# Optimization experiments

Hardware: AMD Instinct MI355X
Metric: run time of the kernel (lower is better)

Reference implementation:

```python
import jax, jax.numpy as jnp
import numpy as np

B, N, N_FEAT = 16, 1024, 128
N_LAYER, AGG_HIDDEN, FC_HIDDEN, N_CLASS = 3, 64, 128, 10
NEG_INF = -9e15
LEAKY_SLOPE = 0.2


def setup_inputs() -> dict:
    key = jax.random.key(0)
    ks = jax.random.split(key, 8)
    x = jax.random.normal(ks[0], (B, N, N_FEAT), dtype=jnp.float32)
    adj = jax.random.randint(ks[1], (B, N, N), 0, 2).astype(jnp.float32)
    # per-layer GAT params, stacked over layers
    Ws = jax.random.normal(ks[2], (N_LAYER, N_FEAT, AGG_HIDDEN), dtype=jnp.float32) * 0.1
    a1 = jax.random.normal(ks[3], (N_LAYER, AGG_HIDDEN), dtype=jnp.float32) * 0.1
    a2 = jax.random.normal(ks[4], (N_LAYER, AGG_HIDDEN), dtype=jnp.float32) * 0.1
    W1 = jax.random.normal(ks[5], (AGG_HIDDEN * N_LAYER, FC_HIDDEN), dtype=jnp.float32) * 0.05
    b1 = jnp.zeros((FC_HIDDEN,), dtype=jnp.float32)
    W2 = jax.random.normal(ks[6], (FC_HIDDEN, N_CLASS), dtype=jnp.float32) * 0.05
    b2 = jnp.zeros((N_CLASS,), dtype=jnp.float32)
    return {"x": x, "adj": adj, "Ws": Ws, "a1": a1, "a2": a2,
            "W1": W1, "b1": b1, "W2": W2, "b2": b2}


def _gat_layer(x, adj, W, a1, a2):
    # h: [B, N, H]
    h = jnp.einsum('bnf,fh->bnh', x, W)
    # e_ij = LeakyReLU(a1.h_i + a2.h_j)  -- split-a trick, avoids [B,N,N,2H]
    f1 = jnp.einsum('bnh,h->bn', h, a1)
    f2 = jnp.einsum('bnh,h->bn', h, a2)
    e = jax.nn.leaky_relu(f1[:, :, None] + f2[:, None, :], LEAKY_SLOPE)  # [B,N,N]
    att = jax.nn.softmax(jnp.where(adj > 0, e, NEG_INF), axis=-1)
    return jnp.einsum('bnm,bmh->bnh', att, h)


def reference(x, adj, Ws, a1, a2, W1, b1, W2, b2):
    # eval mode: dropout is identity
    outs = [jax.nn.relu(_gat_layer(x, adj, Ws[i], a1[i], a2[i]))
            for i in range(N_LAYER)]
    h = jnp.concatenate(outs, axis=2)          # [B, N, H*L]
    pooled = jnp.mean(h, axis=1)               # 'avg' pool over nodes -> [B, H*L]
    z = jax.nn.relu(pooled @ W1 + b1)
    return jax.nn.softmax(z @ W2 + b2, axis=-1)  # [B, n_class]
```

## Files before the change

kernel.cpp:

```cpp
#include <hip/hip_runtime.h>

#define B 16
#define N 1024
#define NF 128
#define NL 3
#define AH 64
#define HC 192
#define FCH 128
#define NC 10
#define L2E 1.44269504088896f

typedef __attribute__((ext_vector_type(8))) short bf16x8;
typedef __attribute__((ext_vector_type(4))) float f32x4;
typedef __attribute__((ext_vector_type(4))) unsigned int u32x4;

static __device__ __forceinline__ unsigned short f2bf(float f) {
  unsigned int x = __builtin_bit_cast(unsigned int, f);
  return (unsigned short)((x + 0x7fffu + ((x >> 16) & 1u)) >> 16);
}
static __device__ __forceinline__ float bf2f(unsigned short u) {
  unsigned int x = ((unsigned int)u) << 16;
  return __builtin_bit_cast(float, x);
}

__global__ __launch_bounds__(256) void k_feat(
    const float* __restrict__ x, const float* __restrict__ Ws,
    const float* __restrict__ a1, const float* __restrict__ a2,
    unsigned short* __restrict__ h_f, float* __restrict__ f1g,
    float* __restrict__ f2g)
{
  __shared__ float xs[64][132];
  __shared__ unsigned short wl[2][64][136];
  unsigned short (*hlds)[72] = (unsigned short(*)[72])&xs[0][0];
  const int t = threadIdx.x;
  const int n0g = blockIdx.x * 64;
  const int gb = n0g >> 10, nl0 = n0g & 1023;
  const int wv = t >> 6, lane = t & 63;
  const int lr = lane & 15, lg = lane >> 4;
  const int lrow = wv * 16 + lr;

  #pragma unroll
  for (int p = 0; p < 8; ++p) {
    const int q = p * 256 + t;
    const int row = q >> 5, c4 = (q & 31) * 4;
    *(float4*)&xs[row][c4] = *(const float4*)&x[(size_t)(n0g + row) * NF + c4];
  }
  __syncthreads();

  bf16x8 xhi[4], xlo[4];
  #pragma unroll
  for (int kf = 0; kf < 4; ++kf) {
    const float4 q0 = *(const float4*)&xs[lrow][kf * 32 + lg * 8];
    const float4 q1 = *(const float4*)&xs[lrow][kf * 32 + lg * 8 + 4];
    const float xv[8] = {q0.x, q0.y, q0.z, q0.w, q1.x, q1.y, q1.z, q1.w};
    #pragma unroll
    for (int e = 0; e < 8; ++e) {
      const unsigned short hi = f2bf(xv[e]);
      xhi[kf][e] = (short)hi;
      xlo[kf][e] = (short)f2bf(xv[e] - bf2f(hi));
    }
  }

  f32x4 acc[12];
  #pragma unroll
  for (int n = 0; n < 12; ++n) acc[n] = (f32x4){0.f, 0.f, 0.f, 0.f};

  for (int l = 0; l < 3; ++l) {
    __syncthreads();
    #pragma unroll
    for (int p = 0; p < 4; ++p) {
      const int task = p * 256 + t;
      const int col = task & 63, oct = task >> 6;
      bf16x8 hv, lv;
      #pragma unroll
      for (int i = 0; i < 8; ++i) {
        const float w = Ws[((size_t)l * NF + oct * 8 + i) * AH + col];
        const unsigned short hi = f2bf(w);
        hv[i] = (short)hi;
        lv[i] = (short)f2bf(w - bf2f(hi));
      }
      *(bf16x8*)&wl[0][col][oct * 8] = hv;
      *(bf16x8*)&wl[1][col][oct * 8] = lv;
    }
    __syncthreads();

    #pragma unroll
    for (int n2 = 0; n2 < 4; ++n2) {
      const int n = l * 4 + n2;
      #pragma unroll
      for (int kf = 0; kf < 4; ++kf) {
        const bf16x8 whi = *(const bf16x8*)&wl[0][n2 * 16 + lr][kf * 32 + lg * 8];
        const bf16x8 wlo = *(const bf16x8*)&wl[1][n2 * 16 + lr][kf * 32 + lg * 8];
        acc[n] = __builtin_amdgcn_mfma_f32_16x16x32_bf16(xhi[kf], whi, acc[n], 0, 0, 0);
        acc[n] = __builtin_amdgcn_mfma_f32_16x16x32_bf16(xhi[kf], wlo, acc[n], 0, 0, 0);
        acc[n] = __builtin_amdgcn_mfma_f32_16x16x32_bf16(xlo[kf], whi, acc[n], 0, 0, 0);
      }
    }
  }

  float s1[3][4], s2[3][4];
  #pragma unroll
  for (int l = 0; l < 3; ++l)
    #pragma unroll
    for (int r = 0; r < 4; ++r) { s1[l][r] = 0.f; s2[l][r] = 0.f; }
  #pragma unroll
  for (int n = 0; n < 12; ++n) {
    const int col = n * 16 + lr;
    const float a1v = a1[col] * L2E, a2v = a2[col] * L2E;
    const int l = n >> 2;
    #pragma unroll
    for (int r = 0; r < 4; ++r) {
      s1[l][r] += acc[n][r] * a1v;
      s2[l][r] += acc[n][r] * a2v;
    }
  }
  #pragma unroll
  for (int off = 1; off < 16; off <<= 1)
    #pragma unroll
    for (int l = 0; l < 3; ++l)
      #pragma unroll
      for (int r = 0; r < 4; ++r) {
        s1[l][r] += __shfl_xor(s1[l][r], off);
        s2[l][r] += __shfl_xor(s2[l][r], off);
      }
  if (lr == 0) {
    #pragma unroll
    for (int l = 0; l < 3; ++l)
      #pragma unroll
      for (int r = 0; r < 4; ++r) {
        const int rw = n0g + wv * 16 + lg * 4 + r;
        f1g[(size_t)l * (B * N) + rw] = s1[l][r];
        f2g[(size_t)l * (B * N) + rw] = s2[l][r];
      }
  }

  __syncthreads();
  #pragma unroll
  for (int n = 0; n < 12; ++n) {
    const int col = n * 16 + lr;
    #pragma unroll
    for (int rp = 0; rp < 2; ++rp) {
      const unsigned int pr = (unsigned int)f2bf(acc[n][rp * 2]) |
                              ((unsigned int)f2bf(acc[n][rp * 2 + 1]) << 16);
      *(unsigned int*)&hlds[col][wv * 16 + lg * 4 + rp * 2] = pr;
    }
  }
  __syncthreads();
  #pragma unroll
  for (int p = 0; p < 6; ++p) {
    const int widx = p * 256 + t;
    const int lane_w = widx & 63;
    const int jb2 = (widx >> 6) & 1;
    const int n_w = (widx >> 7) & 3;
    const int l_w = widx >> 9;
    const int col = l_w * 64 + n_w * 16 + (lane_w & 15);
    const int jloc = jb2 * 32 + (lane_w >> 4) * 8;
    const size_t off =
        ((((size_t)(gb * 3 + l_w) * 4 + n_w) * 32 + (nl0 >> 5) + jb2) * 64 + lane_w) * 8;
    *(uint4*)&h_f[off] = *(const uint4*)&hlds[col][jloc];
  }
}

__global__ __launch_bounds__(192, 3) void k_att(
    const float* __restrict__ adj, const unsigned short* __restrict__ h_f,
    const float* __restrict__ f1, const float* __restrict__ f2,
    float* __restrict__ pooled)
{
  const int bid = blockIdx.x;
  const int blk = (bid & 7) * 128 + (bid >> 3);
  const int b = blk >> 6;
  const int i0 = (blk & 63) * 16;
  const int t = threadIdx.x;
  const int l = t >> 6, lane = t & 63;
  const int lr = lane & 15, lg = lane >> 4;

  __shared__ float uvt[NL][2][N];
  __shared__ unsigned char adjm[2][16][88];

  const float* f2p = f2 + (size_t)l * (B * N) + b * N;
  float mx = -1e30f;
  #pragma unroll
  for (int ch = 0; ch < 4; ++ch) {
    const int jb = ch * 256 + lane * 4;
    const float4 q = *(const float4*)&f2p[jb];
    mx = fmaxf(mx, fmaxf(fmaxf(q.x, q.y), fmaxf(q.z, q.w)));
    *(float4*)&uvt[l][0][jb] =
        (float4){exp2f(q.x), exp2f(q.y), exp2f(q.z), exp2f(q.w)};
    *(float4*)&uvt[l][1][jb] =
        (float4){exp2f(0.2f * q.x), exp2f(0.2f * q.y), exp2f(0.2f * q.z), exp2f(0.2f * q.w)};
  }
  #pragma unroll
  for (int off = 1; off < 64; off <<= 1) mx = fmaxf(mx, __shfl_xor(mx, off));

  const float f1r = f1[(size_t)l * (B * N) + b * N + i0 + lr];
  const float tts = f1r + mx;
  const float sr = fmaxf(tts, 0.f) + 0.2f * fminf(tts, 0.f);
  const float A = exp2f(f1r - sr);
  const float C = exp2f(0.2f * f1r - sr);

  const float* adjb = adj + ((size_t)(b * N + i0)) * N;
  const unsigned short* hfb = h_f + ((size_t)(b * 3 + l)) * 65536;
  const float* ut = &uvt[l][0][0];
  const float* vt = &uvt[l][1][0];
  const bf16x8 ones = {(short)0x3F80, (short)0x3F80, (short)0x3F80, (short)0x3F80,
                       (short)0x3F80, (short)0x3F80, (short)0x3F80, (short)0x3F80};

  const int s_r0 = t >> 4, s_c0 = (t & 15) * 4;
  const int s_r1 = (t + 192) >> 4, s_c1 = ((t + 192) & 15) * 4;

  f32x4 acc[4];
  #pragma unroll
  for (int n = 0; n < 4; ++n) acc[n] = (f32x4){0.f, 0.f, 0.f, 0.f};
  f32x4 accd = (f32x4){0.f, 0.f, 0.f, 0.f};

#define PACK4(U) (((U).x ? 1u : 0u) | ((U).y ? 0x100u : 0u) | \
                  ((U).z ? 0x10000u : 0u) | ((U).w ? 0x1000000u : 0u))

#define STAGE_ISSUE(S0, S1, J) {                                              \
    const int jn = (J) & (N - 1);                                             \
    S0 = *(const uint4*)&adjb[(size_t)s_r0 * N + jn + s_c0];                  \
    if (t < 64) S1 = *(const uint4*)&adjb[(size_t)s_r1 * N + jn + s_c1];      \
  }
#define STAGE_WRITE(S0, S1, SB) {                                             \
    *(unsigned int*)&adjm[SB][s_r0][s_c0] = PACK4(S0);                        \
    if (t < 64) *(unsigned int*)&adjm[SB][s_r1][s_c1] = PACK4(S1);            \
  }

#define LOADJ(BUF, J) {                                                       \
    const int jj = (J) & (N - 1);                                             \
    _Pragma("unroll")                                                         \
    for (int q = 0; q < 8; ++q) {                                             \
      const int ks = q >> 2, n = q & 3;                                       \
      BUF[q] = *(const bf16x8*)&hfb[(((size_t)n * 32 + (jj >> 5) + ks) * 64 + \
                                     lane) * 8];                              \
    } }

#define COMPJ(BUF, SB, J) {                                                   \
    _Pragma("unroll")                                                         \
    for (int ks = 0; ks < 2; ++ks) {                                          \
      const int kb = (J) + ks * 32 + lg * 8;                                  \
      const float4 u0 = *(const float4*)&ut[kb];                              \
      const float4 u1 = *(const float4*)&ut[kb + 4];                          \
      const float4 v0 = *(const float4*)&vt[kb];                              \
      const float4 v1 = *(const float4*)&vt[kb + 4];                          \
      const uint2 mw = *(const uint2*)&adjm[SB][lr][ks * 32 + lg * 8];        \
      const float uu[8] = {u0.x, u0.y, u0.z, u0.w, u1.x, u1.y, u1.z, u1.w};   \
      const float vv[8] = {v0.x, v0.y, v0.z, v0.w, v1.x, v1.y, v1.z, v1.w};   \
      unsigned int pk[4];                                                     \
      _Pragma("unroll")                                                       \
      for (int ep = 0; ep < 4; ++ep) {                                        \
        unsigned int pr[2];                                                   \
        _Pragma("unroll")                                                     \
        for (int h = 0; h < 2; ++h) {                                         \
          const int e = ep * 2 + h;                                           \
          const unsigned int mby =                                            \
              ((e < 4 ? mw.x : mw.y) >> ((e & 3) * 8)) & 0xffu;               \
                \
          const float p = fmaxf(A * uu[e], C * vv[e]) * (float)mby;           \
          pr[h] = __builtin_bit_cast(unsigned int, p) + 0x8000u;              \
        }                                                                     \
        pk[ep] = __builtin_amdgcn_perm(pr[1], pr[0], 0x07060302u);            \
      }                                                                       \
      const u32x4 pkv = {pk[0], pk[1], pk[2], pk[3]};                         \
      const bf16x8 av = __builtin_bit_cast(bf16x8, pkv);                      \
      _Pragma("unroll")                                                       \
      for (int n = 0; n < 4; ++n)                                             \
        acc[n] = __builtin_amdgcn_mfma_f32_16x16x32_bf16(av, BUF[ks * 4 + n], \
                                                         acc[n], 0, 0, 0);    \
      accd = __builtin_amdgcn_mfma_f32_16x16x32_bf16(av, ones, accd, 0, 0, 0);\
    } }

  bf16x8 bA[8], bB[8];
  uint4 SA0, SA1, SB0, SB1;

  STAGE_ISSUE(SA0, SA1, 0);
  STAGE_ISSUE(SB0, SB1, 64);
  LOADJ(bA, 0);
  STAGE_WRITE(SA0, SA1, 0);
  __syncthreads();

  for (int j0 = 0; j0 < N; j0 += 128) {
    STAGE_ISSUE(SA0, SA1, j0 + 128);
    LOADJ(bB, j0 + 64);
    __builtin_amdgcn_sched_barrier(0);
    COMPJ(bA, 0, j0);
    __builtin_amdgcn_sched_barrier(0);
    STAGE_WRITE(SB0, SB1, 1);
    __syncthreads();
    STAGE_ISSUE(SB0, SB1, j0 + 192);
    LOADJ(bA, j0 + 128);
    __builtin_amdgcn_sched_barrier(0);
    COMPJ(bB, 1, j0 + 64);
    __builtin_amdgcn_sched_barrier(0);
    STAGE_WRITE(SA0, SA1, 0);
    __syncthreads();
  }
#undef PACK4
#undef STAGE_ISSUE
#undef STAGE_WRITE
#undef LOADJ
#undef COMPJ

  float dn[4];
  #pragma unroll
  for (int r = 0; r < 4; ++r) dn[r] = 1.f / fmaxf(accd[r], 1e-37f);

  #pragma unroll
  for (int n = 0; n < 4; ++n) {
    float csum = 0.f;
    #pragma unroll
    for (int r = 0; r < 4; ++r) csum += fmaxf(acc[n][r] * dn[r], 0.f);
    csum += __shfl_xor(csum, 16);
    csum += __shfl_xor(csum, 32);
    if (lg == 0) atomicAdd(&pooled[b * HC + l * 64 + n * 16 + lr], csum);
  }
}

__global__ __launch_bounds__(192) void k_head(
    const float* __restrict__ pooled_sums, const float* __restrict__ W1,
    const float* __restrict__ b1, const float* __restrict__ W2,
    const float* __restrict__ b2, float* __restrict__ out)
{
  const int b = blockIdx.x, t = threadIdx.x;
  __shared__ float pooled[HC];
  __shared__ float z[FCH];
  __shared__ float logits[NC];

  if (t < HC) pooled[t] = pooled_sums[b * HC + t] * (1.f / (float)N);
  __syncthreads();

  if (t < FCH) {
    float a = b1[t];
    #pragma unroll 4
    for (int f = 0; f < HC; ++f) a += pooled[f] * W1[(size_t)f * FCH + t];
    z[t] = a > 0.f ? a : 0.f;
  }
  __syncthreads();

  if (t < NC) {
    float a = b2[t];
    #pragma unroll 4
    for (int f = 0; f < FCH; ++f) a += z[f] * W2[(size_t)f * NC + t];
    logits[t] = a;
  }
  __syncthreads();

  if (t == 0) {
    float mxl = logits[0];
    for (int c = 1; c < NC; ++c) mxl = fmaxf(mxl, logits[c]);
    float e[NC], sum = 0.f;
    for (int c = 0; c < NC; ++c) { e[c] = __expf(logits[c] - mxl); sum += e[c]; }
    const float inv = 1.f / sum;
    for (int c = 0; c < NC; ++c) out[b * NC + c] = e[c] * inv;
  }
}

extern "C" void kernel_launch(void* const* d_in, const int* in_sizes, int n_in,
                              void* d_out, int out_size, void* d_ws, size_t ws_size,
                              hipStream_t stream)
{
  const float* x   = (const float*)d_in[0];
  const float* adj = (const float*)d_in[1];
  const float* Ws  = (const float*)d_in[2];
  const float* a1  = (const float*)d_in[3];
  const float* a2  = (const float*)d_in[4];
  const float* W1  = (const float*)d_in[5];
  const float* b1  = (const float*)d_in[6];
  const float* W2  = (const float*)d_in[7];
  const float* b2  = (const float*)d_in[8];
  float* out = (float*)d_out;

  unsigned short* h_f   = (unsigned short*)d_ws;
  float*          f1    = (float*)(h_f + (size_t)B * HC * N);
  float*          f2    = f1 + (size_t)NL * B * N;
  float*          pooled= f2 + (size_t)NL * B * N;

  hipMemsetAsync(pooled, 0, (size_t)B * HC * sizeof(float), stream);
  k_feat<<<256, 256, 0, stream>>>(x, Ws, a1, a2, h_f, f1, f2);
  k_att <<<1024, 192, 0, stream>>>(adj, h_f, f1, f2, pooled);
  k_head<<<B, 192, 0, stream>>>(pooled, W1, b1, W2, b2, out);
}
```

Measured before the change: 71.61 us.

## Prefetch weights across layers and widen adjacency staging with 16-bit masks

In the feature kernel, the next layer's weights are loaded into registers while the current layer's MFMAs run, and occupancy is hinted at two blocks per SM. In the attention kernel, adjacency is staged in 128-column tiles as 16-bit all-ones or zero masks, so masking becomes a bitwise AND on the packed bf16 pair instead of a float multiply. Each block also starts its column sweep at a different phase to spread global memory traffic. This halves the number of barriers per column sweep but uses more registers for the staging and weight buffers and more LDS for the mask tile.

```diff
diff --git a/kernel.cpp b/kernel.cpp
--- a/kernel.cpp
+++ b/kernel.cpp
@@ -23,7 +23,7 @@
   return __builtin_bit_cast(float, x);
 }
 
-__global__ __launch_bounds__(256) void k_feat(
+__global__ __launch_bounds__(256, 2) void k_feat(
     const float* __restrict__ x, const float* __restrict__ Ws,
     const float* __restrict__ a1, const float* __restrict__ a2,
     unsigned short* __restrict__ h_f, float* __restrict__ f1g,
@@ -38,6 +38,46 @@
   const int wv = t >> 6, lane = t & 63;
   const int lr = lane & 15, lg = lane >> 4;
   const int lrow = wv * 16 + lr;
+  const int wcol = t & 63, woct = t >> 6;
+
+#define LOADW(R, L) {                                                         \
+    _Pragma("unroll")                                                         \
+    for (int p = 0; p < 4; ++p) {                                             \
+      const int oct = p * 4 + woct;                                           \
+      _Pragma("unroll")                                                       \
+      for (int i = 0; i < 8; ++i)                                             \
+        R[p][i] = Ws[((size_t)(L) * NF + oct * 8 + i) * AH + wcol];           \
+    } }
+#define WRITEW(R) {                                                           \
+    _Pragma("unroll")                                                         \
+    for (int p = 0; p < 4; ++p) {                                             \
+      const int oct = p * 4 + woct;                                           \
+      bf16x8 hv, lv;                                                          \
+      _Pragma("unroll")                                                       \
+      for (int i = 0; i < 8; ++i) {                                           \
+        const unsigned short hi = f2bf(R[p][i]);                              \
+        hv[i] = (short)hi;                                                    \
+        lv[i] = (short)f2bf(R[p][i] - bf2f(hi));                              \
+      }                                                                       \
+      *(bf16x8*)&wl[0][wcol][oct * 8] = hv;                                   \
+      *(bf16x8*)&wl[1][wcol][oct * 8] = lv;                                   \
+    } }
+#define MFMAL(L) {                                                            \
+    _Pragma("unroll")                                                         \
+    for (int n2 = 0; n2 < 4; ++n2) {                                          \
+      const int n = (L) * 4 + n2;                                             \
+      _Pragma("unroll")                                                       \
+      for (int kf = 0; kf < 4; ++kf) {                                        \
+        const bf16x8 whi = *(const bf16x8*)&wl[0][n2 * 16 + lr][kf * 32 + lg * 8]; \
+        const bf16x8 wlo = *(const bf16x8*)&wl[1][n2 * 16 + lr][kf * 32 + lg * 8]; \
+        acc[n] = __builtin_amdgcn_mfma_f32_16x16x32_bf16(xhi[kf], whi, acc[n], 0, 0, 0); \
+        acc[n] = __builtin_amdgcn_mfma_f32_16x16x32_bf16(xhi[kf], wlo, acc[n], 0, 0, 0); \
+        acc[n] = __builtin_amdgcn_mfma_f32_16x16x32_bf16(xlo[kf], whi, acc[n], 0, 0, 0); \
+      }                                                                       \
+    } }
+
+  float wrA[4][8], wrB[4][8];
+  LOADW(wrA, 0);
 
   #pragma unroll
   for (int p = 0; p < 8; ++p) {
@@ -65,38 +105,23 @@
   #pragma unroll
   for (int n = 0; n < 12; ++n) acc[n] = (f32x4){0.f, 0.f, 0.f, 0.f};
 
-  for (int l = 0; l < 3; ++l) {
-    __syncthreads();
-    #pragma unroll
-    for (int p = 0; p < 4; ++p) {
-      const int task = p * 256 + t;
-      const int col = task & 63, oct = task >> 6;
-      bf16x8 hv, lv;
-      #pragma unroll
-      for (int i = 0; i < 8; ++i) {
-        const float w = Ws[((size_t)l * NF + oct * 8 + i) * AH + col];
-        const unsigned short hi = f2bf(w);
-        hv[i] = (short)hi;
-        lv[i] = (short)f2bf(w - bf2f(hi));
-      }
-      *(bf16x8*)&wl[0][col][oct * 8] = hv;
-      *(bf16x8*)&wl[1][col][oct * 8] = lv;
-    }
-    __syncthreads();
-
-    #pragma unroll
-    for (int n2 = 0; n2 < 4; ++n2) {
-      const int n = l * 4 + n2;
-      #pragma unroll
-      for (int kf = 0; kf < 4; ++kf) {
-        const bf16x8 whi = *(const bf16x8*)&wl[0][n2 * 16 + lr][kf * 32 + lg * 8];
-        const bf16x8 wlo = *(const bf16x8*)&wl[1][n2 * 16 + lr][kf * 32 + lg * 8];
-        acc[n] = __builtin_amdgcn_mfma_f32_16x16x32_bf16(xhi[kf], whi, acc[n], 0, 0, 0);
-        acc[n] = __builtin_amdgcn_mfma_f32_16x16x32_bf16(xhi[kf], wlo, acc[n], 0, 0, 0);
-        acc[n] = __builtin_amdgcn_mfma_f32_16x16x32_bf16(xlo[kf], whi, acc[n], 0, 0, 0);
-      }
-    }
-  }
+  WRITEW(wrA);
+  LOADW(wrB, 1);
+  __syncthreads();
+  MFMAL(0);
+  __syncthreads();
+  WRITEW(wrB);
+  LOADW(wrA, 2);
+  __syncthreads();
+  MFMAL(1);
+  __syncthreads();
+  WRITEW(wrA);
+  __syncthreads();
+  MFMAL(2);
+
+#undef LOADW
+#undef WRITEW
+#undef MFMAL
 
   float s1[3][4], s2[3][4];
   #pragma unroll
@@ -170,12 +195,13 @@
   const int blk = (bid & 7) * 128 + (bid >> 3);
   const int b = blk >> 6;
   const int i0 = (blk & 63) * 16;
+  const int ph = ((bid * 5) & 7) * 128;
   const int t = threadIdx.x;
   const int l = t >> 6, lane = t & 63;
   const int lr = lane & 15, lg = lane >> 4;
 
   __shared__ float uvt[NL][2][N];
-  __shared__ unsigned char adjm[2][16][88];
+  __shared__ unsigned short adjm[2][16][136];
 
   const float* f2p = f2 + (size_t)l * (B * N) + b * N;
   float mx = -1e30f;
@@ -205,25 +231,28 @@
   const bf16x8 ones = {(short)0x3F80, (short)0x3F80, (short)0x3F80, (short)0x3F80,
                        (short)0x3F80, (short)0x3F80, (short)0x3F80, (short)0x3F80};
 
-  const int s_r0 = t >> 4, s_c0 = (t & 15) * 4;
-  const int s_r1 = (t + 192) >> 4, s_c1 = ((t + 192) & 15) * 4;
+  const int s_r = t >> 5, s_c = (t & 31) * 4;
 
   f32x4 acc[4];
   #pragma unroll
   for (int n = 0; n < 4; ++n) acc[n] = (f32x4){0.f, 0.f, 0.f, 0.f};
   f32x4 accd = (f32x4){0.f, 0.f, 0.f, 0.f};
 
-#define PACK4(U) (((U).x ? 1u : 0u) | ((U).y ? 0x100u : 0u) | \
-                  ((U).z ? 0x10000u : 0u) | ((U).w ? 0x1000000u : 0u))
-
-#define STAGE_ISSUE(S0, S1, J) {                                              \
+#define PACK2(X, Y) (((X) ? 0xFFFFu : 0u) | ((Y) ? 0xFFFF0000u : 0u))
+
+#define ISSUE(S0, S1, S2, J) {                                                \
     const int jn = (J) & (N - 1);                                             \
-    S0 = *(const uint4*)&adjb[(size_t)s_r0 * N + jn + s_c0];                  \
-    if (t < 64) S1 = *(const uint4*)&adjb[(size_t)s_r1 * N + jn + s_c1];      \
-  }
-#define STAGE_WRITE(S0, S1, SB) {                                             \
-    *(unsigned int*)&adjm[SB][s_r0][s_c0] = PACK4(S0);                        \
-    if (t < 64) *(unsigned int*)&adjm[SB][s_r1][s_c1] = PACK4(S1);            \
+    S0 = *(const uint4*)&adjb[(size_t)s_r * N + jn + s_c];                    \
+    S1 = *(const uint4*)&adjb[(size_t)(s_r + 6) * N + jn + s_c];              \
+    if (t < 128) S2 = *(const uint4*)&adjb[(size_t)(s_r + 12) * N + jn + s_c];\
+  }
+#define WRITEM(S0, S1, S2, SB) {                                              \
+    *(uint2*)&adjm[SB][s_r][s_c] =                                            \
+        (uint2){PACK2(S0.x, S0.y), PACK2(S0.z, S0.w)};                        \
+    *(uint2*)&adjm[SB][s_r + 6][s_c] =                                        \
+        (uint2){PACK2(S1.x, S1.y), PACK2(S1.z, S1.w)};                        \
+    if (t < 128) *(uint2*)&adjm[SB][s_r + 12][s_c] =                          \
+        (uint2){PACK2(S2.x, S2.y), PACK2(S2.z, S2.w)};                        \
   }
 
 #define LOADJ(BUF, J) {                                                       \
@@ -235,17 +264,18 @@
                                      lane) * 8];                              \
     } }
 
-#define COMPJ(BUF, SB, J) {                                                   \
+#define COMPJ(BUF, SB, J, TOFF) {                                             \
     _Pragma("unroll")                                                         \
     for (int ks = 0; ks < 2; ++ks) {                                          \
-      const int kb = (J) + ks * 32 + lg * 8;                                  \
+      const int kb = ((J) & (N - 1)) + ks * 32 + lg * 8;                      \
       const float4 u0 = *(const float4*)&ut[kb];                              \
       const float4 u1 = *(const float4*)&ut[kb + 4];                          \
       const float4 v0 = *(const float4*)&vt[kb];                              \
       const float4 v1 = *(const float4*)&vt[kb + 4];                          \
-      const uint2 mw = *(const uint2*)&adjm[SB][lr][ks * 32 + lg * 8];        \
+      const uint4 mk = *(const uint4*)&adjm[SB][lr][(TOFF) + ks * 32 + lg * 8];\
       const float uu[8] = {u0.x, u0.y, u0.z, u0.w, u1.x, u1.y, u1.z, u1.w};   \
       const float vv[8] = {v0.x, v0.y, v0.z, v0.w, v1.x, v1.y, v1.z, v1.w};   \
+      const unsigned int mka[4] = {mk.x, mk.y, mk.z, mk.w};                   \
       unsigned int pk[4];                                                     \
       _Pragma("unroll")                                                       \
       for (int ep = 0; ep < 4; ++ep) {                                        \
@@ -253,13 +283,11 @@
         _Pragma("unroll")                                                     \
         for (int h = 0; h < 2; ++h) {                                         \
           const int e = ep * 2 + h;                                           \
-          const unsigned int mby =                                            \
-              ((e < 4 ? mw.x : mw.y) >> ((e & 3) * 8)) & 0xffu;               \
-                \
-          const float p = fmaxf(A * uu[e], C * vv[e]) * (float)mby;           \
+                  \
+          const float p = fmaxf(A * uu[e], C * vv[e]);                        \
           pr[h] = __builtin_bit_cast(unsigned int, p) + 0x8000u;              \
         }                                                                     \
-        pk[ep] = __builtin_amdgcn_perm(pr[1], pr[0], 0x07060302u);            \
+        pk[ep] = __builtin_amdgcn_perm(pr[1], pr[0], 0x07060302u) & mka[ep];  \
       }                                                                       \
       const u32x4 pkv = {pk[0], pk[1], pk[2], pk[3]};                         \
       const bf16x8 av = __builtin_bit_cast(bf16x8, pkv);                      \
@@ -270,36 +298,48 @@
       accd = __builtin_amdgcn_mfma_f32_16x16x32_bf16(av, ones, accd, 0, 0, 0);\
     } }
 
+#define SBAR __builtin_amdgcn_sched_barrier(0)
+
   bf16x8 bA[8], bB[8];
-  uint4 SA0, SA1, SB0, SB1;
-
-  STAGE_ISSUE(SA0, SA1, 0);
-  STAGE_ISSUE(SB0, SB1, 64);
-  LOADJ(bA, 0);
-  STAGE_WRITE(SA0, SA1, 0);
-  __syncthreads();
-
-  for (int j0 = 0; j0 < N; j0 += 128) {
-    STAGE_ISSUE(SA0, SA1, j0 + 128);
-    LOADJ(bB, j0 + 64);
-    __builtin_amdgcn_sched_barrier(0);
-    COMPJ(bA, 0, j0);
-    __builtin_amdgcn_sched_barrier(0);
-    STAGE_WRITE(SB0, SB1, 1);
+  uint4 A0, A1, A2, B0, B1, B2;
+
+  ISSUE(A0, A1, A2, ph);
+  WRITEM(A0, A1, A2, 0);
+  ISSUE(A0, A1, A2, ph + 128);
+  LOADJ(bA, ph);
+  __syncthreads();
+
+  for (int s = 0; s < 8; s += 2) {
+    const int jp = ph + s * 128;
+    ISSUE(B0, B1, B2, jp + 256);
+    LOADJ(bB, jp + 64);
+    SBAR;
+    COMPJ(bA, 0, jp, 0);
+    SBAR;
+    LOADJ(bA, jp + 128);
+    SBAR;
+    COMPJ(bB, 0, jp + 64, 64);
+    SBAR;
+    WRITEM(A0, A1, A2, 1);
     __syncthreads();
-    STAGE_ISSUE(SB0, SB1, j0 + 192);
-    LOADJ(bA, j0 + 128);
-    __builtin_amdgcn_sched_barrier(0);
-    COMPJ(bB, 1, j0 + 64);
-    __builtin_amdgcn_sched_barrier(0);
-    STAGE_WRITE(SA0, SA1, 0);
+    ISSUE(A0, A1, A2, jp + 384);
+    LOADJ(bB, jp + 192);
+    SBAR;
+    COMPJ(bA, 1, jp + 128, 0);
+    SBAR;
+    LOADJ(bA, jp + 256);
+    SBAR;
+    COMPJ(bB, 1, jp + 192, 64);
+    SBAR;
+    WRITEM(B0, B1, B2, 0);
     __syncthreads();
   }
-#undef PACK4
-#undef STAGE_ISSUE
-#undef STAGE_WRITE
+#undef PACK2
+#undef ISSUE
+#undef WRITEM
 #undef LOADJ
 #undef COMPJ
+#undef SBAR
 
   float dn[4];
   #pragma unroll
```

Result: no change. 71.06 us (-0.8%).
